# Kernel optimization log

Hardware: AMD Instinct MI355X
Metric: run time of the kernel (lower is better)

## Reference

```python
import jax, jax.numpy as jnp
import numpy as np

NUM_HEADS = 16
HIDDEN = 2048
HEAD_DIM = HIDDEN // NUM_HEADS


def setup_inputs() -> dict:
    key = jax.random.key(0)
    ks = jax.random.split(key, 9)
    B, S, D = 2, 2048, HIDDEN
    s = 0.02
    return {
        "hidden_states": jax.random.normal(ks[0], (B, S, D), jnp.float32),
        "attention_mask": jnp.ones((B, S), jnp.float32),
        "Wq": jax.random.normal(ks[1], (D, D), jnp.float32) * s,
        "bq": jnp.zeros((D,), jnp.float32),
        "Wk": jax.random.normal(ks[2], (D, D), jnp.float32) * s,
        "bk": jnp.zeros((D,), jnp.float32),
        "Wv": jax.random.normal(ks[3], (D, D), jnp.float32) * s,
        "bv": jnp.zeros((D,), jnp.float32),
        "Wo": jax.random.normal(ks[4], (D, D), jnp.float32) * s,
        "bo": jnp.zeros((D,), jnp.float32),
    }


def _split_heads(x, B, S):
    # [B, S, D] -> [B, H, S, hd]
    return x.reshape(B, S, NUM_HEADS, HEAD_DIM).transpose(0, 2, 1, 3)


def reference(hidden_states, attention_mask, Wq, bq, Wk, bk, Wv, bv, Wo, bo):
    B, S, D = hidden_states.shape
    scale = HEAD_DIM ** -0.5
    # Projections (torch Linear: x @ W.T + b); q scaled as in source
    q = (jnp.einsum('bsd,ed->bse', hidden_states, Wq) + bq) * scale
    k = jnp.einsum('bsd,ed->bse', hidden_states, Wk) + bk
    v = jnp.einsum('bsd,ed->bse', hidden_states, Wv) + bv
    q = _split_heads(q, B, S)
    k = _split_heads(k, B, S)
    v = _split_heads(v, B, S)
    # scores: [B, H, S, S]
    scores = jnp.einsum('bhqd,bhkd->bhqk', q, k)
    # 2D mask path: [B, S] -> additive mask broadcast over heads/query
    add_mask = (1.0 - attention_mask)[:, None, None, :] * jnp.finfo(scores.dtype).min
    scores = scores + add_mask
    attn = jax.nn.softmax(scores, axis=-1)
    out = jnp.einsum('bhqk,bhkd->bhqd', attn, v)
    out = out.transpose(0, 2, 1, 3).reshape(B, S, D)
    out = jnp.einsum('bsd,ed->bse', out, Wo) + bo
    return out
```

## Files before the change

kernel.cpp:

```cpp
#include <hip/hip_runtime.h>

typedef unsigned short u16;
typedef unsigned int   u32;
typedef __attribute__((ext_vector_type(8))) short short8;
typedef __attribute__((ext_vector_type(4))) float f32x4;

#define DEVI static __device__ __forceinline__

DEVI u16 f2bf(float f) {
  u32 u = __float_as_uint(f);
  u32 r = (u + 0x7FFFu + ((u >> 16) & 1u)) >> 16;
  return (u16)r;
}

DEVI void gload_lds16(const void* g, void* l) {
  __builtin_amdgcn_global_load_lds(
      (const __attribute__((address_space(1))) void*)g,
      (__attribute__((address_space(3))) void*)l, 16, 0, 0);
}

__global__ void __launch_bounds__(256) cvt_kernel(const float4* __restrict__ src,
                                                  uint4* __restrict__ dst, int n8) {
  int i = blockIdx.x * 256 + threadIdx.x;
  if (i >= n8) return;
  float4 a = src[2 * i], b = src[2 * i + 1];
  uint4 o;
  o.x = (u32)f2bf(a.x) | ((u32)f2bf(a.y) << 16);
  o.y = (u32)f2bf(a.z) | ((u32)f2bf(a.w) << 16);
  o.z = (u32)f2bf(b.x) | ((u32)f2bf(b.y) << 16);
  o.w = (u32)f2bf(b.z) | ((u32)f2bf(b.w) << 16);
  dst[i] = o;
}

__global__ void __launch_bounds__(256) cvt4_kernel(
    const float4* __restrict__ s0, const float4* __restrict__ s1,
    const float4* __restrict__ s2, const float4* __restrict__ s3,
    uint4* __restrict__ d0, uint4* __restrict__ d1,
    uint4* __restrict__ d2, uint4* __restrict__ d3, int n8) {
  int i = blockIdx.x * 256 + threadIdx.x;
  if (i >= n8) return;
  int seg = blockIdx.y;
  const float4* s = (seg == 0) ? s0 : (seg == 1) ? s1 : (seg == 2) ? s2 : s3;
  uint4* d = (seg == 0) ? d0 : (seg == 1) ? d1 : (seg == 2) ? d2 : d3;
  float4 a = s[2 * i], b = s[2 * i + 1];
  uint4 o;
  o.x = (u32)f2bf(a.x) | ((u32)f2bf(a.y) << 16);
  o.y = (u32)f2bf(a.z) | ((u32)f2bf(a.w) << 16);
  o.z = (u32)f2bf(b.x) | ((u32)f2bf(b.y) << 16);
  o.w = (u32)f2bf(b.z) | ((u32)f2bf(b.w) << 16);
  d[i] = o;
}

template <int MODE>
__global__ void __launch_bounds__(256) gemm_bt(
    const u16* __restrict__ A, const u16* __restrict__ Bw, void* __restrict__ Cp,
    const float* __restrict__ bias0, const float* __restrict__ bias1,
    const float* __restrict__ bias2, int ldc) {
  constexpr int K = 2048;
  __shared__ __align__(16) u16 As[128 * 32];
  __shared__ __align__(16) u16 Bs[128 * 32];
  const int tid = threadIdx.x, w = tid >> 6, l = tid & 63;
  const int wm = w >> 1, wn = w & 1;
  const int bm = blockIdx.x, bn = blockIdx.y;
  const char* Ab = (const char*)(A + (size_t)bm * 128 * K);
  const char* Bb = (const char*)(Bw + (size_t)bn * 128 * K);
  f32x4 acc[4][4] = {};
  for (int kt = 0; kt < K / 32; ++kt) {
#pragma unroll
    for (int q = 0; q < 2; ++q) {
      int byteoff = q * 4096 + w * 1024 + l * 16;
      int row = byteoff >> 6, colb = byteoff & 63;
      gload_lds16(Ab + (size_t)row * (K * 2) + kt * 64 + colb,
                  (char*)As + q * 4096 + w * 1024);
      gload_lds16(Bb + (size_t)row * (K * 2) + kt * 64 + colb,
                  (char*)Bs + q * 4096 + w * 1024);
    }
    __syncthreads();
    short8 af[4], bf[4];
#pragma unroll
    for (int mi = 0; mi < 4; ++mi)
      af[mi] = *(const short8*)((const char*)As + (wm * 64 + mi * 16 + (l & 15)) * 64 + (l >> 4) * 16);
#pragma unroll
    for (int ni = 0; ni < 4; ++ni)
      bf[ni] = *(const short8*)((const char*)Bs + (wn * 64 + ni * 16 + (l & 15)) * 64 + (l >> 4) * 16);
#pragma unroll
    for (int mi = 0; mi < 4; ++mi)
#pragma unroll
      for (int ni = 0; ni < 4; ++ni)
        acc[mi][ni] = __builtin_amdgcn_mfma_f32_16x16x32_bf16(af[mi], bf[ni], acc[mi][ni], 0, 0, 0);
    __syncthreads();
  }
#pragma unroll
  for (int mi = 0; mi < 4; ++mi) {
    int grow = bm * 128 + wm * 64 + mi * 16 + ((l >> 4) << 2);
#pragma unroll
    for (int ni = 0; ni < 4; ++ni) {
      int gcol = bn * 128 + wn * 64 + ni * 16 + (l & 15);
#pragma unroll
      for (int j = 0; j < 4; ++j) {
        float v = acc[mi][ni][j];
        if (MODE == 0) {
          int seg = gcol >> 11;
          const float* bp = (seg == 0) ? bias0 : (seg == 1 ? bias1 : bias2);
          v += bp[gcol & 2047];
          if (seg == 0) v *= 0.08838834764831845f;
          ((u16*)Cp)[(size_t)(grow + j) * ldc + gcol] = f2bf(v);
        } else {
          ((float*)Cp)[(size_t)(grow + j) * ldc + gcol] = v + bias0[gcol];
        }
      }
    }
  }
}

__global__ void __launch_bounds__(256, 2) attn_kernel(const u16* __restrict__ qkv,
                                                      const float* __restrict__ amask,
                                                      u16* __restrict__ ctx) {
  __shared__ __align__(16) char KtB[64 * 256];
  __shared__ __align__(16) char VtB[128 * 128];
  __shared__ __align__(16) char PbB[4][2][2048];
  const int tid = threadIdx.x, w = tid >> 6, l = tid & 63;
  const int l15 = l & 15, l4 = l >> 4;
  const int qt = blockIdx.x & 15, h = (blockIdx.x >> 4) & 15, b = (int)(blockIdx.x >> 8);
  const int ld = 6144;
  const int swq = (l15 & 7) << 4;
  short8 qf[2][4];
#pragma unroll
  for (int qg = 0; qg < 2; ++qg) {
    const u16* qp = qkv + (size_t)(b * 2048 + qt * 128 + w * 32 + qg * 16 + l15) * ld + h * 128;
#pragma unroll
    for (int dc = 0; dc < 4; ++dc) qf[qg][dc] = *(const short8*)(qp + dc * 32 + l4 * 8);
  }
  f32x4 o_[2][8] = {};
  float m_[2] = {-INFINITY, -INFINITY}, s_[2] = {0.f, 0.f};
  const u16* kbase = qkv + (size_t)b * 2048 * ld + 2048 + h * 128;
  const u16* vbase = qkv + (size_t)b * 2048 * ld + 4096 + h * 128;
  const float* mbase = amask + b * 2048;
  const int kr = tid >> 2, c0 = (tid & 3) * 32;
  const int kb = (tid & 15) * 4, dvb = (tid >> 4) * 8;
  for (int t = 0; t < 32; ++t) {
    const int k0 = t * 64;
    __syncthreads();
    {
      const u16* kg = kbase + (size_t)(k0 + kr) * ld + c0;
      char* drow = KtB + kr * 256;
      const int sw = (kr & 7) << 4;
#pragma unroll
      for (int u = 0; u < 4; ++u)
        *(uint4*)(drow + ((c0 * 2 + u * 16) ^ sw)) = *(const uint4*)(kg + u * 8);
      uint4 vr[4];
#pragma unroll
      for (int r = 0; r < 4; ++r)
        vr[r] = *(const uint4*)(vbase + (size_t)(k0 + kb + r) * ld + dvb);
#pragma unroll
      for (int dvi = 0; dvi < 8; ++dvi) {
        int dv = dvb + dvi;
        u32 lo = (u32)((const u16*)&vr[0])[dvi] | ((u32)((const u16*)&vr[1])[dvi] << 16);
        u32 hi = (u32)((const u16*)&vr[2])[dvi] | ((u32)((const u16*)&vr[3])[dvi] << 16);
        uint2 pk; pk.x = lo; pk.y = hi;
        *(uint2*)(VtB + dv * 128 + ((kb * 2) ^ ((dv & 7) << 4))) = pk;
      }
    }
    __syncthreads();
    float4 amv[4];
#pragma unroll
    for (int kc = 0; kc < 4; ++kc) {
      float4 mv = *(const float4*)(mbase + k0 + kc * 16 + l4 * 4);
      amv[kc].x = (1.0f - mv.x) * -3.402823466e38f;
      amv[kc].y = (1.0f - mv.y) * -3.402823466e38f;
      amv[kc].z = (1.0f - mv.z) * -3.402823466e38f;
      amv[kc].w = (1.0f - mv.w) * -3.402823466e38f;
    }
    f32x4 sA[2][4];
#pragma unroll
    for (int kc = 0; kc < 4; ++kc) {
      const int krow = kc * 16 + l15;
      const char* krp = KtB + krow * 256;
      const int sw = (krow & 7) << 4;
      short8 kf[4];
#pragma unroll
      for (int dc = 0; dc < 4; ++dc)
        kf[dc] = *(const short8*)(krp + ((dc * 64 + l4 * 16) ^ sw));
#pragma unroll
      for (int qg = 0; qg < 2; ++qg) {
        f32x4 tacc = {0.f, 0.f, 0.f, 0.f};
#pragma unroll
        for (int dc = 0; dc < 4; ++dc)
          tacc = __builtin_amdgcn_mfma_f32_16x16x32_bf16(kf[dc], qf[qg][dc], tacc, 0, 0, 0);
        sA[qg][kc] = tacc;
      }
    }
    float fct[2];
#pragma unroll
    for (int qg = 0; qg < 2; ++qg) {
      float pm = -INFINITY;
#pragma unroll
      for (int kc = 0; kc < 4; ++kc) {
        sA[qg][kc][0] += amv[kc].x; sA[qg][kc][1] += amv[kc].y;
        sA[qg][kc][2] += amv[kc].z; sA[qg][kc][3] += amv[kc].w;
#pragma unroll
        for (int j = 0; j < 4; ++j) pm = fmaxf(pm, sA[qg][kc][j]);
      }
      pm = fmaxf(pm, __shfl_xor(pm, 16));
      pm = fmaxf(pm, __shfl_xor(pm, 32));
      float mn = fmaxf(m_[qg], pm);
      fct[qg] = __expf(m_[qg] - mn);
      m_[qg] = mn;
      float rs = 0.f;
#pragma unroll
      for (int kc = 0; kc < 4; ++kc) {
#pragma unroll
        for (int j = 0; j < 4; ++j) {
          float p = __expf(sA[qg][kc][j] - mn);
          rs += p;
          sA[qg][kc][j] = p;
        }
        u32 lo = (u32)f2bf(sA[qg][kc][0]) | ((u32)f2bf(sA[qg][kc][1]) << 16);
        u32 hi = (u32)f2bf(sA[qg][kc][2]) | ((u32)f2bf(sA[qg][kc][3]) << 16);
        uint2 pk; pk.x = lo; pk.y = hi;
        *(uint2*)(PbB[w][qg] + l15 * 128 + ((kc * 32 + l4 * 8) ^ swq)) = pk;
      }
      rs += __shfl_xor(rs, 16);
      rs += __shfl_xor(rs, 32);
      s_[qg] = s_[qg] * fct[qg] + rs;
    }
#pragma unroll
    for (int qg = 0; qg < 2; ++qg) {
      float fq[4];
#pragma unroll
      for (int j = 0; j < 4; ++j) fq[j] = __shfl(fct[qg], l4 * 4 + j);
#pragma unroll
      for (int dvc = 0; dvc < 8; ++dvc)
#pragma unroll
        for (int j = 0; j < 4; ++j) o_[qg][dvc][j] *= fq[j];
    }
    short8 pa[2][2];
#pragma unroll
    for (int qg = 0; qg < 2; ++qg)
#pragma unroll
      for (int kh = 0; kh < 2; ++kh)
        pa[qg][kh] = *(const short8*)(PbB[w][qg] + l15 * 128 + ((kh * 64 + l4 * 16) ^ swq));
#pragma unroll
    for (int dvc = 0; dvc < 8; ++dvc) {
      const int dv = dvc * 16 + l15;
      const char* vrp = VtB + dv * 128;
      const int swv = (dv & 7) << 4;
#pragma unroll
      for (int kh = 0; kh < 2; ++kh) {
        short8 vf = *(const short8*)(vrp + ((kh * 64 + l4 * 16) ^ swv));
#pragma unroll
        for (int qg = 0; qg < 2; ++qg)
          o_[qg][dvc] = __builtin_amdgcn_mfma_f32_16x16x32_bf16(pa[qg][kh], vf, o_[qg][dvc], 0, 0, 0);
      }
    }
  }
#pragma unroll
  for (int qg = 0; qg < 2; ++qg) {
    float inv = 1.0f / s_[qg];
    float iq[4];
#pragma unroll
    for (int j = 0; j < 4; ++j) iq[j] = __shfl(inv, l4 * 4 + j);
    u16* crow = ctx + (size_t)(b * 2048 + qt * 128 + w * 32 + qg * 16 + l4 * 4) * 2048 + h * 128;
#pragma unroll
    for (int dvc = 0; dvc < 8; ++dvc)
#pragma unroll
      for (int j = 0; j < 4; ++j)
        crow[(size_t)j * 2048 + dvc * 16 + l15] = f2bf(o_[qg][dvc][j] * iq[j]);
  }
}

extern "C" void kernel_launch(void* const* d_in, const int* in_sizes, int n_in,
                              void* d_out, int out_size, void* d_ws, size_t ws_size,
                              hipStream_t stream) {
  const float* hs    = (const float*)d_in[0];
  const float* amask = (const float*)d_in[1];
  const float* Wq    = (const float*)d_in[2];
  const float* bq    = (const float*)d_in[3];
  const float* Wk    = (const float*)d_in[4];
  const float* bk    = (const float*)d_in[5];
  const float* Wv    = (const float*)d_in[6];
  const float* bv    = (const float*)d_in[7];
  const float* Wo    = (const float*)d_in[8];
  const float* bo    = (const float*)d_in[9];
  float* out = (float*)d_out;

  char* ws = (char*)d_ws;
  u16* hiddenB = (u16*)ws;
  u16* wcatB   = (u16*)(ws + 16777216ull);
  u16* woB     = (u16*)(ws + 16777216ull + 25165824ull);
  u16* qkvB    = (u16*)(ws + 16777216ull + 25165824ull + 8388608ull);
  u16* ctxB    = (u16*)(ws + 16777216ull + 25165824ull + 8388608ull + 50331648ull);

  cvt_kernel<<<4096, 256, 0, stream>>>((const float4*)hs, (uint4*)hiddenB, 1048576);
  cvt4_kernel<<<dim3(2048, 4), 256, 0, stream>>>(
      (const float4*)Wq, (const float4*)Wk, (const float4*)Wv, (const float4*)Wo,
      (uint4*)wcatB, (uint4*)(wcatB + 2048 * 2048), (uint4*)(wcatB + 2 * 2048 * 2048),
      (uint4*)woB, 524288);

  gemm_bt<0><<<dim3(32, 48), 256, 0, stream>>>(hiddenB, wcatB, qkvB, bq, bk, bv, 6144);
  attn_kernel<<<512, 256, 0, stream>>>(qkvB, amask, ctxB);
  gemm_bt<1><<<dim3(32, 16), 256, 0, stream>>>(ctxB, woB, out, bo, nullptr, nullptr, 2048);
}
```

Baseline: 429.1 us.

## Double-buffer K/V tiles with register prefetch and lazy softmax rescaling

Splits the K/V shared-memory tiles into two buffers. The global loads for the next tile go into registers at the start of each iteration and are written to the other buffer mid-iteration, which hides load latency and removes one barrier per tile. It also skips the running-max rescale of the output accumulator unless the max rises by more than 8 (FA4-style lazy rescaling), and raises wave priority around the MFMA blocks. This costs twice the LDS (which may reduce occupancy at 2 blocks/CU) and more registers for the prefetch.

```diff
diff --git a/kernel.cpp b/kernel.cpp
--- a/kernel.cpp
+++ b/kernel.cpp
@@ -116,8 +116,8 @@
 __global__ void __launch_bounds__(256, 2) attn_kernel(const u16* __restrict__ qkv,
                                                       const float* __restrict__ amask,
                                                       u16* __restrict__ ctx) {
-  __shared__ __align__(16) char KtB[64 * 256];
-  __shared__ __align__(16) char VtB[128 * 128];
+  __shared__ __align__(16) char KtB[2][64 * 256];
+  __shared__ __align__(16) char VtB[2][128 * 128];
   __shared__ __align__(16) char PbB[4][2][2048];
   const int tid = threadIdx.x, w = tid >> 6, l = tid & 63;
   const int l15 = l & 15, l4 = l >> 4;
@@ -138,30 +138,40 @@
   const float* mbase = amask + b * 2048;
   const int kr = tid >> 2, c0 = (tid & 3) * 32;
   const int kb = (tid & 15) * 4, dvb = (tid >> 4) * 8;
+  uint4 kreg[4], vreg[4];
+
+  auto load_regs = [&](int t) {
+    const u16* kg = kbase + (size_t)(t * 64 + kr) * ld + c0;
+#pragma unroll
+    for (int u = 0; u < 4; ++u) kreg[u] = *(const uint4*)(kg + u * 8);
+#pragma unroll
+    for (int r = 0; r < 4; ++r)
+      vreg[r] = *(const uint4*)(vbase + (size_t)(t * 64 + kb + r) * ld + dvb);
+  };
+  auto write_lds = [&](int buf) {
+    char* drow = KtB[buf] + kr * 256;
+    const int sw = (kr & 7) << 4;
+#pragma unroll
+    for (int u = 0; u < 4; ++u)
+      *(uint4*)(drow + ((c0 * 2 + u * 16) ^ sw)) = kreg[u];
+#pragma unroll
+    for (int dvi = 0; dvi < 8; ++dvi) {
+      int dv = dvb + dvi;
+      u32 lo = (u32)((const u16*)&vreg[0])[dvi] | ((u32)((const u16*)&vreg[1])[dvi] << 16);
+      u32 hi = (u32)((const u16*)&vreg[2])[dvi] | ((u32)((const u16*)&vreg[3])[dvi] << 16);
+      uint2 pk; pk.x = lo; pk.y = hi;
+      *(uint2*)(VtB[buf] + dv * 128 + ((kb * 2) ^ ((dv & 7) << 4))) = pk;
+    }
+  };
+
+  load_regs(0);
+  write_lds(0);
+  __syncthreads();
+
   for (int t = 0; t < 32; ++t) {
+    const int cur = t & 1;
     const int k0 = t * 64;
-    __syncthreads();
-    {
-      const u16* kg = kbase + (size_t)(k0 + kr) * ld + c0;
-      char* drow = KtB + kr * 256;
-      const int sw = (kr & 7) << 4;
-#pragma unroll
-      for (int u = 0; u < 4; ++u)
-        *(uint4*)(drow + ((c0 * 2 + u * 16) ^ sw)) = *(const uint4*)(kg + u * 8);
-      uint4 vr[4];
-#pragma unroll
-      for (int r = 0; r < 4; ++r)
-        vr[r] = *(const uint4*)(vbase + (size_t)(k0 + kb + r) * ld + dvb);
-#pragma unroll
-      for (int dvi = 0; dvi < 8; ++dvi) {
-        int dv = dvb + dvi;
-        u32 lo = (u32)((const u16*)&vr[0])[dvi] | ((u32)((const u16*)&vr[1])[dvi] << 16);
-        u32 hi = (u32)((const u16*)&vr[2])[dvi] | ((u32)((const u16*)&vr[3])[dvi] << 16);
-        uint2 pk; pk.x = lo; pk.y = hi;
-        *(uint2*)(VtB + dv * 128 + ((kb * 2) ^ ((dv & 7) << 4))) = pk;
-      }
-    }
-    __syncthreads();
+    if (t < 31) load_regs(t + 1);
     float4 amv[4];
 #pragma unroll
     for (int kc = 0; kc < 4; ++kc) {
@@ -172,10 +182,11 @@
       amv[kc].w = (1.0f - mv.w) * -3.402823466e38f;
     }
     f32x4 sA[2][4];
+    __builtin_amdgcn_s_setprio(1);
 #pragma unroll
     for (int kc = 0; kc < 4; ++kc) {
       const int krow = kc * 16 + l15;
-      const char* krp = KtB + krow * 256;
+      const char* krp = KtB[cur] + krow * 256;
       const int sw = (krow & 7) << 4;
       short8 kf[4];
 #pragma unroll
@@ -190,7 +201,7 @@
         sA[qg][kc] = tacc;
       }
     }
-    float fct[2];
+    __builtin_amdgcn_s_setprio(0);
 #pragma unroll
     for (int qg = 0; qg < 2; ++qg) {
       float pm = -INFINITY;
@@ -203,15 +214,25 @@
       }
       pm = fmaxf(pm, __shfl_xor(pm, 16));
       pm = fmaxf(pm, __shfl_xor(pm, 32));
-      float mn = fmaxf(m_[qg], pm);
-      fct[qg] = __expf(m_[qg] - mn);
-      m_[qg] = mn;
+      if (!__all(pm - m_[qg] <= 8.0f)) {
+        float mn = fmaxf(m_[qg], pm);
+        float fct = __expf(m_[qg] - mn);
+        m_[qg] = mn;
+        s_[qg] *= fct;
+        float fq[4];
+#pragma unroll
+        for (int j = 0; j < 4; ++j) fq[j] = __shfl(fct, l4 * 4 + j);
+#pragma unroll
+        for (int dvc = 0; dvc < 8; ++dvc)
+#pragma unroll
+          for (int j = 0; j < 4; ++j) o_[qg][dvc][j] *= fq[j];
+      }
       float rs = 0.f;
 #pragma unroll
       for (int kc = 0; kc < 4; ++kc) {
 #pragma unroll
         for (int j = 0; j < 4; ++j) {
-          float p = __expf(sA[qg][kc][j] - mn);
+          float p = __expf(sA[qg][kc][j] - m_[qg]);
           rs += p;
           sA[qg][kc][j] = p;
         }
@@ -222,28 +243,20 @@
       }
       rs += __shfl_xor(rs, 16);
       rs += __shfl_xor(rs, 32);
-      s_[qg] = s_[qg] * fct[qg] + rs;
-    }
-#pragma unroll
-    for (int qg = 0; qg < 2; ++qg) {
-      float fq[4];
-#pragma unroll
-      for (int j = 0; j < 4; ++j) fq[j] = __shfl(fct[qg], l4 * 4 + j);
-#pragma unroll
-      for (int dvc = 0; dvc < 8; ++dvc)
-#pragma unroll
-        for (int j = 0; j < 4; ++j) o_[qg][dvc][j] *= fq[j];
-    }
+      s_[qg] += rs;
+    }
+    if (t < 31) write_lds(cur ^ 1);
     short8 pa[2][2];
 #pragma unroll
     for (int qg = 0; qg < 2; ++qg)
 #pragma unroll
       for (int kh = 0; kh < 2; ++kh)
         pa[qg][kh] = *(const short8*)(PbB[w][qg] + l15 * 128 + ((kh * 64 + l4 * 16) ^ swq));
+    __builtin_amdgcn_s_setprio(1);
 #pragma unroll
     for (int dvc = 0; dvc < 8; ++dvc) {
       const int dv = dvc * 16 + l15;
-      const char* vrp = VtB + dv * 128;
+      const char* vrp = VtB[cur] + dv * 128;
       const int swv = (dv & 7) << 4;
 #pragma unroll
       for (int kh = 0; kh < 2; ++kh) {
@@ -253,6 +266,8 @@
           o_[qg][dvc] = __builtin_amdgcn_mfma_f32_16x16x32_bf16(pa[qg][kh], vf, o_[qg][dvc], 0, 0, 0);
       }
     }
+    __builtin_amdgcn_s_setprio(0);
+    __syncthreads();
   }
 #pragma unroll
   for (int qg = 0; qg < 2; ++qg) {
```

Result: slower. 444.5 us (+3.6%).
